# Performance work log

Hardware: AMD Instinct MI355X
Metric: run time of the kernel (lower is better)

## Reference

```python
import jax, jax.numpy as jnp
import numpy as np

BN_EPS = 1e-5
NORM_EPS = 1e-12  # F.normalize default eps


def reference(x, conv_w, bn_gamma, bn_beta):
    # 1x1 conv dimension reduction: [B,2048,H,W] -> [B,256,H,W]
    z = jnp.einsum('bchw,dc->bdhw', x, conv_w)
    # BatchNorm2d (training-mode batch statistics) + ReLU
    mu = z.mean(axis=(0, 2, 3), keepdims=True)
    var = z.var(axis=(0, 2, 3), keepdims=True)
    z = (z - mu) / jnp.sqrt(var + BN_EPS)
    z = z * bn_gamma.reshape(1, -1, 1, 1) + bn_beta.reshape(1, -1, 1, 1)
    z = jax.nn.relu(z)

    B, d, h, w = z.shape
    M = h * w
    xm = z.reshape(B, d, M)
    # Covpool: y = x I_hat x^T with I_hat = (I - 11^T/M)/M == centered 2nd moment
    xc = xm - xm.mean(axis=-1, keepdims=True)
    cov = jnp.einsum('bdm,bem->bde', xc, xc) / M  # [B,d,d]

    # Eigen decomposition (cov is symmetric PSD; SVD of PSD == eigh)
    s, U = jnp.linalg.eigh(cov)  # s: [B,d], U: [B,d,d]
    eps = jnp.finfo(cov.dtype).eps
    s = jnp.maximum(s, eps)

    # ExponentialInverse: U exp(-S) U^T
    inv_x = jnp.einsum('bid,bd,bjd->bij', U, jnp.exp(-s), U)
    # Power (matrix sqrt): U S^{1/2} U^T
    out = jnp.einsum('bid,bd,bjd->bij', U, jnp.sqrt(s), U)

    # attention = out @ inv_x^T  (inv_x is symmetric, transpose kept for fidelity)
    att = jnp.einsum('bij,bkj->bik', out, inv_x)
    flat = att.reshape(B, -1)
    nrm = jnp.maximum(jnp.linalg.norm(flat, axis=1, keepdims=True), NORM_EPS)
    normalized = (flat / nrm).reshape(att.shape)
    att = out * (att / normalized)

    y = att + out
    iu = jnp.triu_indices(d)
    return y[:, iu[0], iu[1]]  # [B, d*(d+1)/2]


def setup_inputs() -> dict:
    key = jax.random.key(0)
    k1, k2 = jax.random.split(key)
    x = jax.random.normal(k1, (32, 2048, 28, 28), dtype=jnp.float32)
    # kaiming-normal fan_out scaling for 1x1 conv: std = sqrt(2/fan_out)=sqrt(2/256)
    conv_w = jax.random.normal(k2, (256, 2048), dtype=jnp.float32) * np.sqrt(2.0 / 256.0)
    bn_gamma = jnp.ones((256,), dtype=jnp.float32)
    bn_beta = jnp.zeros((256,), dtype=jnp.float32)
    return {'x': x, 'conv_w': conv_w, 'bn_gamma': bn_gamma, 'bn_beta': bn_beta}
```

## Files before the change

kernel.cpp:

```cpp
#include <hip/hip_runtime.h>


typedef unsigned short u16;
typedef __attribute__((ext_vector_type(8))) short bf16x8;
typedef __attribute__((ext_vector_type(4))) float f32x4;

__device__ __forceinline__ u16 f2bf(float f) {
  unsigned u = __builtin_bit_cast(unsigned, f);
  u += 0x7FFFu + ((u >> 16) & 1u);
  return (u16)(u >> 16);
}
__device__ __forceinline__ float bf2f(u16 h) {
  unsigned u = ((unsigned)h) << 16;
  return __builtin_bit_cast(float, u);
}

__device__ __forceinline__
void mm_core(const u16* __restrict__ Ah, const u16* __restrict__ Al,
             const u16* __restrict__ Bh, const u16* __restrict__ Bl,
             long boff, int row0, int col0,
             u16 (*lds)[128][8][8], f32x4 acc[4][2])
{
  const int tid = threadIdx.x;
  const int wave = tid >> 6, lane = tid & 63;
  const int wm = wave >> 2, wn = wave & 3;
  const int mL = lane & 15, q = lane >> 4;
  const u16* baseA[2] = {Ah + boff, Al + boff};
  const u16* baseB[2] = {Bh + boff, Bl + boff};

  for (int k0 = 0; k0 < 256; k0 += 64) {
    __syncthreads();
#pragma unroll
    for (int it = 0; it < 8; ++it) {
      const int t = it >> 1;
      const int r = ((it & 1) << 9) + tid;
      const int m = r >> 3, c = r & 7;
      const u16* src = (t < 2 ? baseA[t] : baseB[t - 2])
                     + (long)((t < 2 ? row0 : col0) + m) * 256 + k0 + c * 8;
      *reinterpret_cast<uint4*>(&lds[t][m][c ^ (m & 7)][0]) =
          *reinterpret_cast<const uint4*>(src);
    }
    __syncthreads();
#pragma unroll
    for (int kk = 0; kk < 2; ++kk) {
      bf16x8 ah[4], al[4], bh[2], bl[2];
#pragma unroll
      for (int i = 0; i < 4; ++i) {
        const int ma = wm * 64 + i * 16 + mL;
        const int ca = (kk * 4 + q) ^ (ma & 7);
        ah[i] = *reinterpret_cast<const bf16x8*>(&lds[0][ma][ca][0]);
        al[i] = *reinterpret_cast<const bf16x8*>(&lds[1][ma][ca][0]);
      }
#pragma unroll
      for (int j = 0; j < 2; ++j) {
        const int nb = wn * 32 + j * 16 + mL;
        const int cb = (kk * 4 + q) ^ (nb & 7);
        bh[j] = *reinterpret_cast<const bf16x8*>(&lds[2][nb][cb][0]);
        bl[j] = *reinterpret_cast<const bf16x8*>(&lds[3][nb][cb][0]);
      }
#pragma unroll
      for (int i = 0; i < 4; ++i)
#pragma unroll
        for (int j = 0; j < 2; ++j) {
          acc[i][j] = __builtin_amdgcn_mfma_f32_16x16x32_bf16(ah[i], bh[j], acc[i][j], 0, 0, 0);
          acc[i][j] = __builtin_amdgcn_mfma_f32_16x16x32_bf16(ah[i], bl[j], acc[i][j], 0, 0, 0);
          acc[i][j] = __builtin_amdgcn_mfma_f32_16x16x32_bf16(al[i], bh[j], acc[i][j], 0, 0, 0);
        }
    }
  }
}

template<int MB>
__global__ __launch_bounds__(512)
void fuse_k(const u16* __restrict__ A0, const u16* __restrict__ B0, u16* __restrict__ C0,
            float al0, float b10, float dg0, const float* __restrict__ cf0,
            const u16* __restrict__ A1, const u16* __restrict__ B1, u16* __restrict__ C1,
            u16* __restrict__ D1, float al1, float b11, float dg1,
            float hc1, float hc2, float hc3, const float* __restrict__ cf1, long LO)
{
  __shared__ u16 lds[4][128][8][8];
  int z = blockIdx.z;
  const bool hB = (z >= 32);
  const u16 *Ah, *Bh; u16 *C, *D = nullptr;
  float al, b1, dg; const float* cf;
  if (!hB) { Ah = A0; Bh = B0; C = C0; al = al0; b1 = b10; dg = dg0; cf = cf0; }
  else { z -= 32; Ah = A1; Bh = B1; C = C1; D = D1; al = al1; b1 = b11; dg = dg1; cf = cf1; }
  const long boff = (long)z * 65536;
  const int row0 = blockIdx.y * 128, col0 = blockIdx.x * 128;
  const int wave = threadIdx.x >> 6, lane = threadIdx.x & 63;
  const int wm = wave >> 2, wn = wave & 3;
  const int mL = lane & 15, q = lane >> 4;

  f32x4 acc[4][2];
#pragma unroll
  for (int i = 0; i < 4; ++i)
#pragma unroll
    for (int j = 0; j < 2; ++j) acc[i][j] = {0.f, 0.f, 0.f, 0.f};

  mm_core(Ah, Ah + LO, Bh, Bh + LO, boff, row0, col0, lds, acc);

#pragma unroll
  for (int i = 0; i < 4; ++i) {
    const int rbase = row0 + wm * 64 + i * 16 + q * 4;
#pragma unroll
    for (int j = 0; j < 2; ++j) {
      const int cc = col0 + wn * 32 + j * 16 + mL;
#pragma unroll
      for (int rg = 0; rg < 4; ++rg) {
        const int rr = rbase + rg;
        const long o = boff + (long)rr * 256 + cc;
        const float vr = acc[i][j][rg];
        if (MB == 1 && hB) {
          u16 h = f2bf(vr);
          C[o] = h; C[o + LO] = f2bf(vr - bf2f(h));
          float hv = fmaf(vr, hc1, cf[o] * hc2);
          if (rr == cc) hv += hc3;
          h = f2bf(hv);
          D[o] = h; D[o + LO] = f2bf(hv - bf2f(h));
        } else {
          float v = al * vr;
          if (cf) v = fmaf(b1, cf[o], v);
          if (rr == cc) v += dg;
          const u16 h = f2bf(v);
          C[o] = h; C[o + LO] = f2bf(v - bf2f(h));
        }
      }
    }
  }
}

__global__ __launch_bounds__(512)
void gemm2_pair_k(const u16* __restrict__ A0, const u16* __restrict__ B0, u16* __restrict__ C0,
                  const u16* __restrict__ A1, const u16* __restrict__ B1, u16* __restrict__ C1,
                  long LO)
{
  __shared__ u16 lds[4][128][8][8];
  int z = blockIdx.z;
  const u16 *Ah, *Bh; u16* Chp;
  if (z < 32) { Ah = A0; Bh = B0; Chp = C0; }
  else { z -= 32; Ah = A1; Bh = B1; Chp = C1; }
  const long boff = (long)z * 65536;
  const int row0 = blockIdx.y * 128, col0 = blockIdx.x * 128;
  const int wave = threadIdx.x >> 6, lane = threadIdx.x & 63;
  const int wm = wave >> 2, wn = wave & 3;
  const int mL = lane & 15, q = lane >> 4;

  f32x4 acc[4][2];
#pragma unroll
  for (int i = 0; i < 4; ++i)
#pragma unroll
    for (int j = 0; j < 2; ++j) acc[i][j] = {0.f, 0.f, 0.f, 0.f};

  mm_core(Ah, Ah + LO, Bh, Bh + LO, boff, row0, col0, lds, acc);

#pragma unroll
  for (int i = 0; i < 4; ++i) {
    const int rbase = row0 + wm * 64 + i * 16 + q * 4;
#pragma unroll
    for (int j = 0; j < 2; ++j) {
      const int cc = col0 + wn * 32 + j * 16 + mL;
#pragma unroll
      for (int rg = 0; rg < 4; ++rg) {
        const long o = boff + (long)(rbase + rg) * 256 + cc;
        const float v = acc[i][j][rg];
        const u16 h = f2bf(v);
        Chp[o] = h; Chp[o + LO] = f2bf(v - bf2f(h));
      }
    }
  }
}

template<int MODE>
__global__ __launch_bounds__(512)
void gemmN64_k(const u16* __restrict__ Ah, const u16* __restrict__ Al,
               const u16* __restrict__ Bh, const u16* __restrict__ Bl,
               u16* __restrict__ Ch, u16* __restrict__ Cl,
               const float* __restrict__ cf, float alpha, float b1, float diag,
               float* __restrict__ attn2)
{
  __shared__ u16 ldsA[2][128][8][8];
  __shared__ u16 ldsB[2][64][8][8];
  const long boff = (long)blockIdx.z * 65536;
  const int row0 = blockIdx.y * 128, col0 = blockIdx.x * 64;
  const int tid = threadIdx.x;
  const int wave = tid >> 6, lane = tid & 63;
  const int wm = wave >> 1, wn = wave & 1;
  const int mL = lane & 15, q = lane >> 4;
  const u16* baseA[2] = {Ah + boff, Al + boff};
  const u16* baseB[2] = {Bh + boff, Bl + boff};

  f32x4 acc[2][2];
#pragma unroll
  for (int i = 0; i < 2; ++i)
#pragma unroll
    for (int j = 0; j < 2; ++j) acc[i][j] = {0.f, 0.f, 0.f, 0.f};

  for (int k0 = 0; k0 < 256; k0 += 64) {
    __syncthreads();
#pragma unroll
    for (int it = 0; it < 4; ++it) {
      const int t = it >> 1;
      const int r = ((it & 1) << 9) + tid;
      const int m = r >> 3, c = r & 7;
      *reinterpret_cast<uint4*>(&ldsA[t][m][c ^ (m & 7)][0]) =
          *reinterpret_cast<const uint4*>(baseA[t] + (long)(row0 + m) * 256 + k0 + c * 8);
    }
#pragma unroll
    for (int it = 0; it < 2; ++it) {
      const int m = tid >> 3, c = tid & 7;
      *reinterpret_cast<uint4*>(&ldsB[it][m][c ^ (m & 7)][0]) =
          *reinterpret_cast<const uint4*>(baseB[it] + (long)(col0 + m) * 256 + k0 + c * 8);
    }
    __syncthreads();
#pragma unroll
    for (int kk = 0; kk < 2; ++kk) {
      bf16x8 ah[2], alo[2], bh[2], bl[2];
#pragma unroll
      for (int i = 0; i < 2; ++i) {
        const int ma = wm * 32 + i * 16 + mL;
        const int ca = (kk * 4 + q) ^ (ma & 7);
        ah[i]  = *reinterpret_cast<const bf16x8*>(&ldsA[0][ma][ca][0]);
        alo[i] = *reinterpret_cast<const bf16x8*>(&ldsA[1][ma][ca][0]);
      }
#pragma unroll
      for (int j = 0; j < 2; ++j) {
        const int nb = wn * 32 + j * 16 + mL;
        const int cb = (kk * 4 + q) ^ (nb & 7);
        bh[j] = *reinterpret_cast<const bf16x8*>(&ldsB[0][nb][cb][0]);
        bl[j] = *reinterpret_cast<const bf16x8*>(&ldsB[1][nb][cb][0]);
      }
#pragma unroll
      for (int i = 0; i < 2; ++i)
#pragma unroll
        for (int j = 0; j < 2; ++j) {
          acc[i][j] = __builtin_amdgcn_mfma_f32_16x16x32_bf16(ah[i],  bh[j], acc[i][j], 0, 0, 0);
          acc[i][j] = __builtin_amdgcn_mfma_f32_16x16x32_bf16(ah[i],  bl[j], acc[i][j], 0, 0, 0);
          acc[i][j] = __builtin_amdgcn_mfma_f32_16x16x32_bf16(alo[i], bh[j], acc[i][j], 0, 0, 0);
        }
    }
  }

  if (MODE == 2) {
    float ssum = 0.f;
#pragma unroll
    for (int i = 0; i < 2; ++i)
#pragma unroll
      for (int j = 0; j < 2; ++j)
#pragma unroll
        for (int rg = 0; rg < 4; ++rg) ssum = fmaf(acc[i][j][rg], acc[i][j][rg], ssum);
#pragma unroll
    for (int o = 32; o > 0; o >>= 1) ssum += __shfl_down(ssum, o);
    __syncthreads();
    float* red = (float*)&ldsA[0][0][0][0];
    if (lane == 0) red[wave] = ssum;
    __syncthreads();
    if (tid == 0) {
      float t8 = 0.f;
#pragma unroll
      for (int wv = 0; wv < 8; ++wv) t8 += red[wv];
      atomicAdd(attn2 + blockIdx.z, t8);
    }
    return;
  }

#pragma unroll
  for (int i = 0; i < 2; ++i) {
    const int rbase = row0 + wm * 32 + i * 16 + q * 4;
#pragma unroll
    for (int j = 0; j < 2; ++j) {
      const int cc = col0 + wn * 32 + j * 16 + mL;
#pragma unroll
      for (int rg = 0; rg < 4; ++rg) {
        const int rr = rbase + rg;
        const long o = boff + (long)rr * 256 + cc;
        float v = alpha * acc[i][j][rg];
        if (cf) v = fmaf(b1, cf[o], v);
        if (rr == cc) v += diag;
        const u16 h = f2bf(v);
        Ch[o] = h; Cl[o] = f2bf(v - bf2f(h));
      }
    }
  }
}

__global__ __launch_bounds__(512)
void conv_k(const u16* __restrict__ wb, const float* __restrict__ x,
            float* __restrict__ z0, float* __restrict__ z1)
{
  __shared__ u16 ldsA[256][8][8];
  __shared__ u16 ldsB[64][8][8];
  const int tid = threadIdx.x;
  const int b = blockIdx.z;
  const int n0 = blockIdx.x * 64;
  const int ks = blockIdx.y;
  const int kb0 = ks * 1024;
  const int wave = tid >> 6, lane = tid & 63;
  const int wm = wave >> 1, wn = wave & 1;
  const int mL = lane & 15, q = lane >> 4;
  const float* xb = x + (long)b * 2048 * 784;
  float* zp = (ks == 0 ? z0 : z1);

  f32x4 acc[4][2];
#pragma unroll
  for (int i = 0; i < 4; ++i)
#pragma unroll
    for (int j = 0; j < 2; ++j) acc[i][j] = {0.f, 0.f, 0.f, 0.f};

  const int kc = tid >> 6, nc = tid & 63;
  const int gn = n0 + nc;
  const bool nok = (gn < 784);

  for (int k0 = 0; k0 < 1024; k0 += 64) {
    const int kg = kb0 + k0;
    __syncthreads();
#pragma unroll
    for (int it = 0; it < 4; ++it) {
      const int g = it * 512 + tid;
      const int m = g >> 3, c = g & 7;
      *reinterpret_cast<uint4*>(&ldsA[m][c ^ (m & 7)][0]) =
          *reinterpret_cast<const uint4*>(wb + (long)m * 2048 + kg + c * 8);
    }
    {
      float vv[8];
#pragma unroll
      for (int jk = 0; jk < 8; ++jk)
        vv[jk] = nok ? xb[(long)(kg + kc * 8 + jk) * 784 + gn] : 0.f;
      ushort4 ua, ub;
      ua.x = f2bf(vv[0]); ua.y = f2bf(vv[1]); ua.z = f2bf(vv[2]); ua.w = f2bf(vv[3]);
      ub.x = f2bf(vv[4]); ub.y = f2bf(vv[5]); ub.z = f2bf(vv[6]); ub.w = f2bf(vv[7]);
      const int ch = kc ^ (nc & 7);
      *reinterpret_cast<ushort4*>(&ldsB[nc][ch][0]) = ua;
      *reinterpret_cast<ushort4*>(&ldsB[nc][ch][4]) = ub;
    }
    __syncthreads();
#pragma unroll
    for (int kk = 0; kk < 2; ++kk) {
      bf16x8 af[4], bfv[2];
#pragma unroll
      for (int i = 0; i < 4; ++i) {
        const int ma = wm * 64 + i * 16 + mL;
        af[i] = *reinterpret_cast<const bf16x8*>(&ldsA[ma][(kk * 4 + q) ^ (ma & 7)][0]);
      }
#pragma unroll
      for (int j = 0; j < 2; ++j) {
        const int nb = wn * 32 + j * 16 + mL;
        bfv[j] = *reinterpret_cast<const bf16x8*>(&ldsB[nb][(kk * 4 + q) ^ (nb & 7)][0]);
      }
#pragma unroll
      for (int i = 0; i < 4; ++i)
#pragma unroll
        for (int j = 0; j < 2; ++j)
          acc[i][j] = __builtin_amdgcn_mfma_f32_16x16x32_bf16(af[i], bfv[j], acc[i][j], 0, 0, 0);
    }
  }
#pragma unroll
  for (int i = 0; i < 4; ++i) {
    const int rbase = wm * 64 + i * 16 + q * 4;
#pragma unroll
    for (int j = 0; j < 2; ++j) {
      const int cc = n0 + wn * 32 + j * 16 + mL;
      if (cc >= 784) continue;
#pragma unroll
      for (int rg = 0; rg < 4; ++rg)
        zp[((long)b * 256 + rbase + rg) * 784 + cc] = acc[i][j][rg];
    }
  }
}

__global__ __launch_bounds__(512)
void gram_k(const u16* __restrict__ zb, const float* __restrict__ rs,
            float* __restrict__ cov, u16* __restrict__ C2h, u16* __restrict__ C2l)
{
  __shared__ u16 ldsA[128][8][8];
  __shared__ u16 ldsB[64][8][8];
  const int tid = threadIdx.x;
  const int b = blockIdx.z;
  const int col0 = blockIdx.x * 64, row0 = blockIdx.y * 128;
  const int wave = tid >> 6, lane = tid & 63;
  const int wm = wave >> 1, wn = wave & 1;
  const int mL = lane & 15, q = lane >> 4;
  const u16* zbb = zb + (long)b * 256 * 832;

  f32x4 acc[2][2];
#pragma unroll
  for (int i = 0; i < 2; ++i)
#pragma unroll
    for (int j = 0; j < 2; ++j) acc[i][j] = {0.f, 0.f, 0.f, 0.f};

  for (int k0 = 0; k0 < 832; k0 += 64) {
    __syncthreads();
#pragma unroll
    for (int it = 0; it < 2; ++it) {
      const int r = it * 512 + tid;
      const int m = r >> 3, c = r & 7;
      *reinterpret_cast<uint4*>(&ldsA[m][c ^ (m & 7)][0]) =
          *reinterpret_cast<const uint4*>(zbb + (long)(row0 + m) * 832 + k0 + c * 8);
    }
    {
      const int m = tid >> 3, c = tid & 7;
      *reinterpret_cast<uint4*>(&ldsB[m][c ^ (m & 7)][0]) =
          *reinterpret_cast<const uint4*>(zbb + (long)(col0 + m) * 832 + k0 + c * 8);
    }
    __syncthreads();
#pragma unroll
    for (int kk = 0; kk < 2; ++kk) {
      bf16x8 af[2], bfv[2];
#pragma unroll
      for (int i = 0; i < 2; ++i) {
        const int ma = wm * 32 + i * 16 + mL;
        af[i] = *reinterpret_cast<const bf16x8*>(&ldsA[ma][(kk * 4 + q) ^ (ma & 7)][0]);
      }
#pragma unroll
      for (int j = 0; j < 2; ++j) {
        const int nb = wn * 32 + j * 16 + mL;
        bfv[j] = *reinterpret_cast<const bf16x8*>(&ldsB[nb][(kk * 4 + q) ^ (nb & 7)][0]);
      }
#pragma unroll
      for (int i = 0; i < 2; ++i)
#pragma unroll
        for (int j = 0; j < 2; ++j)
          acc[i][j] = __builtin_amdgcn_mfma_f32_16x16x32_bf16(af[i], bfv[j], acc[i][j], 0, 0, 0);
    }
  }
  const float inv_m = 1.f / 784.f;
#pragma unroll
  for (int i = 0; i < 2; ++i) {
    const int rr0 = row0 + wm * 32 + i * 16 + q * 4;
#pragma unroll
    for (int j = 0; j < 2; ++j) {
      const int cc = col0 + wn * 32 + j * 16 + mL;
      const float mu_c = rs[b * 256 + cc] * inv_m;
#pragma unroll
      for (int rg = 0; rg < 4; ++rg) {
        const int rr = rr0 + rg;
        const float mu_r = rs[b * 256 + rr] * inv_m;
        const long o = ((long)b * 256 + rr) * 256 + cc;
        const float cv = fmaf(acc[i][j][rg], inv_m, -mu_r * mu_c);
        cov[o] = cv;
        const u16 h = f2bf(cv);
        C2h[o] = h; C2l[o] = f2bf(cv - bf2f(h));
      }
    }
  }
}

__global__ __launch_bounds__(256)
void bn_stats_k(const float* __restrict__ z0, const float* __restrict__ z1,
                float* __restrict__ ps, float* __restrict__ pq)
{
  const int d = blockIdx.x, sl = blockIdx.y, t = threadIdx.x;
  const int lane = t & 63, wid = t >> 6;
  __shared__ float ws[4], wq[4];
  float s = 0.f, qq = 0.f;
  for (int b = sl * 4; b < sl * 4 + 4; ++b) {
    const long off = ((long)b * 256 + d) * 784;
    for (int m = t; m < 784; m += 256) {
      const float v = z0[off + m] + z1[off + m];
      s += v; qq = fmaf(v, v, qq);
    }
  }
#pragma unroll
  for (int o = 32; o > 0; o >>= 1) { s += __shfl_down(s, o); qq += __shfl_down(qq, o); }
  if (lane == 0) { ws[wid] = s; wq[wid] = qq; }
  __syncthreads();
  if (t == 0) {
    ps[d * 8 + sl] = ws[0] + ws[1] + ws[2] + ws[3];
    pq[d * 8 + sl] = wq[0] + wq[1] + wq[2] + wq[3];
  }
}

__global__ __launch_bounds__(256)
void bn_apply_k(const float* __restrict__ z0, const float* __restrict__ z1,
                const float* __restrict__ gamma, const float* __restrict__ beta,
                const float* __restrict__ ps, const float* __restrict__ pq,
                u16* __restrict__ zb, float* __restrict__ rs)
{
  const int d = blockIdx.x, b = blockIdx.y, t = threadIdx.x;
  const int lane = t & 63, wid = t >> 6;
  __shared__ float bc[2], ws[4];
  if (t == 0) {
    float sum = 0.f, sq = 0.f;
#pragma unroll
    for (int s8 = 0; s8 < 8; ++s8) { sum += ps[d * 8 + s8]; sq += pq[d * 8 + s8]; }
    const float inv_n = 1.f / 25088.f;
    const float mean = sum * inv_n;
    const float var = sq * inv_n - mean * mean;
    const float sc = gamma[d] * rsqrtf(var + 1e-5f);
    bc[0] = sc; bc[1] = fmaf(-mean, sc, beta[d]);
  }
  __syncthreads();
  const float sc = bc[0], sh = bc[1];
  const long off = ((long)b * 256 + d) * 784;
  u16* qp = zb + ((long)b * 256 + d) * 832;
  float rsum = 0.f;
  for (int m = t; m < 832; m += 256) {
    const float v = (m < 784)
        ? fmaxf(fmaf(z0[off + m] + z1[off + m], sc, sh), 0.f) : 0.f;
    qp[m] = f2bf(v);
    rsum += v;
  }
#pragma unroll
  for (int o = 32; o > 0; o >>= 1) rsum += __shfl_down(rsum, o);
  if (lane == 0) ws[wid] = rsum;
  __syncthreads();
  if (t == 0) rs[b * 256 + d] = ws[0] + ws[1] + ws[2] + ws[3];
}

__global__ __launch_bounds__(1024)
void power_k(const float* __restrict__ cov, float* __restrict__ s,
             float* __restrict__ attn2)
{
  const int b = blockIdx.x, tid = threadIdx.x;
  const int i = tid & 255, g = tid >> 8;
  const float* A = cov + (long)b * 65536;
  __shared__ float v[256];
  __shared__ float part[4][256];
  __shared__ float red[4];
  if (g == 0) v[i] = 1.f;
  __syncthreads();
  float lam = 1.f;
  for (int it = 0; it < 10; ++it) {
    float u = 0.f;
    const int jb = g * 64;
#pragma unroll 8
    for (int j = jb; j < jb + 64; ++j) u = fmaf(A[(long)j * 256 + i], v[j], u);
    part[g][i] = u;
    __syncthreads();
    if (g == 0) {
      u = part[0][i] + part[1][i] + part[2][i] + part[3][i];
      float ss = u * u;
#pragma unroll
      for (int o = 32; o > 0; o >>= 1) ss += __shfl_down(ss, o);
      if ((i & 63) == 0) red[i >> 6] = ss;
    }
    __syncthreads();
    lam = sqrtf(red[0] + red[1] + red[2] + red[3]);
    if (g == 0) v[i] = u / lam;
    __syncthreads();
  }
  if (tid == 0) { s[b] = 1.8f / lam; attn2[b] = 0.f; }
}

__global__ __launch_bounds__(256)
void init_k(const float* __restrict__ cov, const float* __restrict__ s,
            u16* __restrict__ Yh, u16* __restrict__ Yl,
            u16* __restrict__ Th, u16* __restrict__ Tl)
{
  const int b = blockIdx.y, i = blockIdx.x, j = threadIdx.x;
  const long o = ((long)b * 256 + i) * 256 + j;
  const float a = cov[o] * s[b];
  u16 h = f2bf(a);
  Yh[o] = h; Yl[o] = f2bf(a - bf2f(h));
  float tv = -0.5f * a;
  if (i == j) tv += 1.5f;
  h = f2bf(tv);
  Th[o] = h; Tl[o] = f2bf(tv - bf2f(h));
}

__global__ __launch_bounds__(256)
void out_k(const u16* __restrict__ Yh, const u16* __restrict__ Yl,
           const float* __restrict__ s, const float* __restrict__ attn2,
           float* __restrict__ out)
{
  const int i = blockIdx.x, b = blockIdx.y, j = threadIdx.x;
  if (j < i) return;
  const float inv = rsqrtf(s[b]);
  const float nrm = fmaxf(sqrtf(fmaxf(attn2[b], 0.f)) * inv, 1e-12f);
  const float scv = inv * (1.f + nrm);
  const long o = ((long)b * 256 + i) * 256 + j;
  const long off = (long)b * 32896 + (long)i * 256 - (long)i * (i - 1) / 2 + (j - i);
  out[off] = (bf2f(Yh[o]) + bf2f(Yl[o])) * scv;
}

__global__ __launch_bounds__(256)
void cast_w_k(const float* __restrict__ w, u16* __restrict__ wb)
{
  const int idx = blockIdx.x * 256 + threadIdx.x;
  wb[idx] = f2bf(w[idx]);
}

extern "C" void kernel_launch(void* const* d_in, const int* in_sizes, int n_in,
                              void* d_out, int out_size, void* d_ws, size_t ws_size,
                              hipStream_t stream)
{
  const float* x     = (const float*)d_in[0];
  const float* w     = (const float*)d_in[1];
  const float* gamma = (const float*)d_in[2];
  const float* beta  = (const float*)d_in[3];
  float* out = (float*)d_out;

  const long PS = 4194304;
  const long LO = 2097152;
  u16* S[9];
  for (int k = 0; k < 9; ++k) S[k] = (u16*)d_ws + (long)k * PS;
  char* base = (char*)d_ws;
  float* z0  = (float*)(base + 75497472);
  float* z1  = (float*)(base + 101187584);
  u16*   zb  = (u16*)(base + 126877696);
  float* cov = (float*)(base + 140509184);
  u16*   wbuf = (u16*)(base + 140509184);
  float* st  = (float*)(base + 148897792);
  float* sv = st, *attn2 = st + 32, *rs = st + 64;
  float* ps = st + 64 + 8192, *pq = ps + 2048;
  u16 *C2 = S[5], *V = S[6], *Ha = S[7], *Hb = S[8];

  const dim3 blk(256), blk5(512);
  const dim3 gP(2, 2, 64);
  const dim3 gT(4, 2, 32);
  const dim3 gE(256, 32);

  cast_w_k<<<dim3(2048), blk, 0, stream>>>(w, wbuf);
  conv_k<<<dim3(13, 2, 32), blk5, 0, stream>>>(wbuf, x, z0, z1);
  bn_stats_k<<<dim3(256, 8), blk, 0, stream>>>(z0, z1, ps, pq);
  bn_apply_k<<<dim3(256, 32), blk, 0, stream>>>(z0, z1, gamma, beta, ps, pq, zb, rs);
  gram_k<<<gT, blk5, 0, stream>>>(zb, rs, cov, C2, C2 + LO);
  power_k<<<dim3(32), dim3(1024), 0, stream>>>(cov, sv, attn2);
  init_k<<<gE, blk, 0, stream>>>(cov, sv, S[0], S[0] + LO, S[1], S[1] + LO);

  fuse_k<1><<<gP, blk5, 0, stream>>>(
      S[0], S[1], S[2], 1.f, 0.f, 0.f, (const float*)nullptr,
      C2, C2, V, Ha, 1.f, 0.f, 0.f,
      1.f / 40320.f, -1.f / 5040.f, 1.f / 720.f, cov, LO);

  int iY = 2, iZ = 1, fa = 0, fb = 3, fc = 4;
  for (int it = 1; it <= 7; ++it) {
    const int iT = fa;
    if (it == 1)
      fuse_k<0><<<gP, blk5, 0, stream>>>(
          S[iZ], S[iY], S[iT], -0.5f, 0.f, 1.5f, (const float*)nullptr,
          V, Ha, Hb, (u16*)nullptr, 1.f, -1.f / 120.f, 1.f / 24.f,
          0.f, 0.f, 0.f, cov, LO);
    else if (it == 2)
      fuse_k<0><<<gP, blk5, 0, stream>>>(
          S[iZ], S[iY], S[iT], -0.5f, 0.f, 1.5f, (const float*)nullptr,
          V, Hb, Ha, (u16*)nullptr, 1.f, -1.f / 6.f, 0.5f,
          0.f, 0.f, 0.f, cov, LO);
    else if (it == 3)
      fuse_k<0><<<gP, blk5, 0, stream>>>(
          S[iZ], S[iY], S[iT], -0.5f, 0.f, 1.5f, (const float*)nullptr,
          V, Ha, Hb, (u16*)nullptr, 1.f, -1.f, 1.f,
          0.f, 0.f, 0.f, cov, LO);
    else
      gemmN64_k<0><<<gT, blk5, 0, stream>>>(
          S[iZ], S[iZ] + LO, S[iY], S[iY] + LO, S[iT], S[iT] + LO,
          (const float*)nullptr, -0.5f, 0.f, 1.5f, (float*)nullptr);
    if (it < 7) {
      gemm2_pair_k<<<gP, blk5, 0, stream>>>(S[iY], S[iT], S[fb],
                                            S[iT], S[iZ], S[fc], LO);
      const int nY = fb, nZ = fc;
      fa = iY; fb = iZ; fc = iT;
      iY = nY; iZ = nZ;
    } else {
      gemmN64_k<0><<<gT, blk5, 0, stream>>>(
          S[iY], S[iY] + LO, S[iT], S[iT] + LO, S[fb], S[fb] + LO,
          (const float*)nullptr, 1.f, 0.f, 0.f, (float*)nullptr);
      iY = fb;
    }
  }

  gemmN64_k<2><<<gT, blk5, 0, stream>>>(
      S[iY], S[iY] + LO, Hb, Hb + LO, (u16*)nullptr, (u16*)nullptr,
      (const float*)nullptr, 1.f, 0.f, 0.f, attn2);
  out_k<<<gE, blk, 0, stream>>>(S[iY], S[iY] + LO, sv, attn2, out);
}
```

Measured before the change: 681.1 us.

## Shrink fused GEMM tiles, software-pipeline conv gather, vectorize BN kernels

```diff
diff --git a/kernel.cpp b/kernel.cpp
--- a/kernel.cpp
+++ b/kernel.cpp
@@ -15,70 +15,16 @@
   return __builtin_bit_cast(float, u);
 }
 
-__device__ __forceinline__
-void mm_core(const u16* __restrict__ Ah, const u16* __restrict__ Al,
-             const u16* __restrict__ Bh, const u16* __restrict__ Bl,
-             long boff, int row0, int col0,
-             u16 (*lds)[128][8][8], f32x4 acc[4][2])
-{
-  const int tid = threadIdx.x;
-  const int wave = tid >> 6, lane = tid & 63;
-  const int wm = wave >> 2, wn = wave & 3;
-  const int mL = lane & 15, q = lane >> 4;
-  const u16* baseA[2] = {Ah + boff, Al + boff};
-  const u16* baseB[2] = {Bh + boff, Bl + boff};
-
-  for (int k0 = 0; k0 < 256; k0 += 64) {
-    __syncthreads();
-#pragma unroll
-    for (int it = 0; it < 8; ++it) {
-      const int t = it >> 1;
-      const int r = ((it & 1) << 9) + tid;
-      const int m = r >> 3, c = r & 7;
-      const u16* src = (t < 2 ? baseA[t] : baseB[t - 2])
-                     + (long)((t < 2 ? row0 : col0) + m) * 256 + k0 + c * 8;
-      *reinterpret_cast<uint4*>(&lds[t][m][c ^ (m & 7)][0]) =
-          *reinterpret_cast<const uint4*>(src);
-    }
-    __syncthreads();
-#pragma unroll
-    for (int kk = 0; kk < 2; ++kk) {
-      bf16x8 ah[4], al[4], bh[2], bl[2];
-#pragma unroll
-      for (int i = 0; i < 4; ++i) {
-        const int ma = wm * 64 + i * 16 + mL;
-        const int ca = (kk * 4 + q) ^ (ma & 7);
-        ah[i] = *reinterpret_cast<const bf16x8*>(&lds[0][ma][ca][0]);
-        al[i] = *reinterpret_cast<const bf16x8*>(&lds[1][ma][ca][0]);
-      }
-#pragma unroll
-      for (int j = 0; j < 2; ++j) {
-        const int nb = wn * 32 + j * 16 + mL;
-        const int cb = (kk * 4 + q) ^ (nb & 7);
-        bh[j] = *reinterpret_cast<const bf16x8*>(&lds[2][nb][cb][0]);
-        bl[j] = *reinterpret_cast<const bf16x8*>(&lds[3][nb][cb][0]);
-      }
-#pragma unroll
-      for (int i = 0; i < 4; ++i)
-#pragma unroll
-        for (int j = 0; j < 2; ++j) {
-          acc[i][j] = __builtin_amdgcn_mfma_f32_16x16x32_bf16(ah[i], bh[j], acc[i][j], 0, 0, 0);
-          acc[i][j] = __builtin_amdgcn_mfma_f32_16x16x32_bf16(ah[i], bl[j], acc[i][j], 0, 0, 0);
-          acc[i][j] = __builtin_amdgcn_mfma_f32_16x16x32_bf16(al[i], bh[j], acc[i][j], 0, 0, 0);
-        }
-    }
-  }
-}
-
 template<int MB>
 __global__ __launch_bounds__(512)
-void fuse_k(const u16* __restrict__ A0, const u16* __restrict__ B0, u16* __restrict__ C0,
-            float al0, float b10, float dg0, const float* __restrict__ cf0,
-            const u16* __restrict__ A1, const u16* __restrict__ B1, u16* __restrict__ C1,
-            u16* __restrict__ D1, float al1, float b11, float dg1,
-            float hc1, float hc2, float hc3, const float* __restrict__ cf1, long LO)
-{
-  __shared__ u16 lds[4][128][8][8];
+void fuseN64_k(const u16* __restrict__ A0, const u16* __restrict__ B0, u16* __restrict__ C0,
+               float al0, float b10, float dg0, const float* __restrict__ cf0,
+               const u16* __restrict__ A1, const u16* __restrict__ B1, u16* __restrict__ C1,
+               u16* __restrict__ D1, float al1, float b11, float dg1,
+               float hc1, float hc2, float hc3, const float* __restrict__ cf1, long LO)
+{
+  __shared__ u16 ldsA[2][128][8][8];
+  __shared__ u16 ldsB[2][64][8][8];
   int z = blockIdx.z;
   const bool hB = (z >= 32);
   const u16 *Ah, *Bh; u16 *C, *D = nullptr;
@@ -86,22 +32,68 @@
   if (!hB) { Ah = A0; Bh = B0; C = C0; al = al0; b1 = b10; dg = dg0; cf = cf0; }
   else { z -= 32; Ah = A1; Bh = B1; C = C1; D = D1; al = al1; b1 = b11; dg = dg1; cf = cf1; }
   const long boff = (long)z * 65536;
-  const int row0 = blockIdx.y * 128, col0 = blockIdx.x * 128;
-  const int wave = threadIdx.x >> 6, lane = threadIdx.x & 63;
-  const int wm = wave >> 2, wn = wave & 3;
+  const int row0 = blockIdx.y * 128, col0 = blockIdx.x * 64;
+  const int tid = threadIdx.x;
+  const int wave = tid >> 6, lane = tid & 63;
+  const int wm = wave >> 1, wn = wave & 1;
   const int mL = lane & 15, q = lane >> 4;
-
-  f32x4 acc[4][2];
-#pragma unroll
-  for (int i = 0; i < 4; ++i)
+  const u16* baseA[2] = {Ah + boff, Ah + LO + boff};
+  const u16* baseB[2] = {Bh + boff, Bh + LO + boff};
+
+  f32x4 acc[2][2];
+#pragma unroll
+  for (int i = 0; i < 2; ++i)
 #pragma unroll
     for (int j = 0; j < 2; ++j) acc[i][j] = {0.f, 0.f, 0.f, 0.f};
 
-  mm_core(Ah, Ah + LO, Bh, Bh + LO, boff, row0, col0, lds, acc);
-
-#pragma unroll
-  for (int i = 0; i < 4; ++i) {
-    const int rbase = row0 + wm * 64 + i * 16 + q * 4;
+  for (int k0 = 0; k0 < 256; k0 += 64) {
+    __syncthreads();
+#pragma unroll
+    for (int it = 0; it < 4; ++it) {
+      const int t = it >> 1;
+      const int r = ((it & 1) << 9) + tid;
+      const int m = r >> 3, c = r & 7;
+      *reinterpret_cast<uint4*>(&ldsA[t][m][c ^ (m & 7)][0]) =
+          *reinterpret_cast<const uint4*>(baseA[t] + (long)(row0 + m) * 256 + k0 + c * 8);
+    }
+#pragma unroll
+    for (int it = 0; it < 2; ++it) {
+      const int m = tid >> 3, c = tid & 7;
+      *reinterpret_cast<uint4*>(&ldsB[it][m][c ^ (m & 7)][0]) =
+          *reinterpret_cast<const uint4*>(baseB[it] + (long)(col0 + m) * 256 + k0 + c * 8);
+    }
+    __syncthreads();
+#pragma unroll
+    for (int kk = 0; kk < 2; ++kk) {
+      bf16x8 ah[2], alo[2], bh[2], bl[2];
+#pragma unroll
+      for (int i = 0; i < 2; ++i) {
+        const int ma = wm * 32 + i * 16 + mL;
+        const int ca = (kk * 4 + q) ^ (ma & 7);
+        ah[i]  = *reinterpret_cast<const bf16x8*>(&ldsA[0][ma][ca][0]);
+        alo[i] = *reinterpret_cast<const bf16x8*>(&ldsA[1][ma][ca][0]);
+      }
+#pragma unroll
+      for (int j = 0; j < 2; ++j) {
+        const int nb = wn * 32 + j * 16 + mL;
+        const int cb = (kk * 4 + q) ^ (nb & 7);
+        bh[j] = *reinterpret_cast<const bf16x8*>(&ldsB[0][nb][cb][0]);
+        bl[j] = *reinterpret_cast<const bf16x8*>(&ldsB[1][nb][cb][0]);
+      }
+#pragma unroll
+      for (int i = 0; i < 2; ++i)
+#pragma unroll
+        for (int j = 0; j < 2; ++j) {
+          acc[i][j] = __builtin_amdgcn_mfma_f32_16x16x32_bf16(ah[i],  bh[j], acc[i][j], 0, 0, 0);
+          acc[i][j] = __builtin_amdgcn_mfma_f32_16x16x32_bf16(ah[i],  bl[j], acc[i][j], 0, 0, 0);
+          acc[i][j] = __builtin_amdgcn_mfma_f32_16x16x32_bf16(alo[i], bh[j], acc[i][j], 0, 0, 0);
+        }
+    }
+  }
+
+#pragma unroll
+  for (int i = 0; i < 2; ++i) {
+    const int rbase = row0 + wm * 32 + i * 16 + q * 4;
 #pragma unroll
     for (int j = 0; j < 2; ++j) {
       const int cc = col0 + wn * 32 + j * 16 + mL;
@@ -129,47 +121,6 @@
   }
 }
 
-__global__ __launch_bounds__(512)
-void gemm2_pair_k(const u16* __restrict__ A0, const u16* __restrict__ B0, u16* __restrict__ C0,
-                  const u16* __restrict__ A1, const u16* __restrict__ B1, u16* __restrict__ C1,
-                  long LO)
-{
-  __shared__ u16 lds[4][128][8][8];
-  int z = blockIdx.z;
-  const u16 *Ah, *Bh; u16* Chp;
-  if (z < 32) { Ah = A0; Bh = B0; Chp = C0; }
-  else { z -= 32; Ah = A1; Bh = B1; Chp = C1; }
-  const long boff = (long)z * 65536;
-  const int row0 = blockIdx.y * 128, col0 = blockIdx.x * 128;
-  const int wave = threadIdx.x >> 6, lane = threadIdx.x & 63;
-  const int wm = wave >> 2, wn = wave & 3;
-  const int mL = lane & 15, q = lane >> 4;
-
-  f32x4 acc[4][2];
-#pragma unroll
-  for (int i = 0; i < 4; ++i)
-#pragma unroll
-    for (int j = 0; j < 2; ++j) acc[i][j] = {0.f, 0.f, 0.f, 0.f};
-
-  mm_core(Ah, Ah + LO, Bh, Bh + LO, boff, row0, col0, lds, acc);
-
-#pragma unroll
-  for (int i = 0; i < 4; ++i) {
-    const int rbase = row0 + wm * 64 + i * 16 + q * 4;
-#pragma unroll
-    for (int j = 0; j < 2; ++j) {
-      const int cc = col0 + wn * 32 + j * 16 + mL;
-#pragma unroll
-      for (int rg = 0; rg < 4; ++rg) {
-        const long o = boff + (long)(rbase + rg) * 256 + cc;
-        const float v = acc[i][j][rg];
-        const u16 h = f2bf(v);
-        Chp[o] = h; Chp[o + LO] = f2bf(v - bf2f(h));
-      }
-    }
-  }
-}
-
 template<int MODE>
 __global__ __launch_bounds__(512)
 void gemmN64_k(const u16* __restrict__ Ah, const u16* __restrict__ Al,
@@ -292,13 +243,12 @@
   const int tid = threadIdx.x;
   const int b = blockIdx.z;
   const int n0 = blockIdx.x * 64;
-  const int ks = blockIdx.y;
-  const int kb0 = ks * 1024;
+  const int kb0 = blockIdx.y * 1024;
   const int wave = tid >> 6, lane = tid & 63;
   const int wm = wave >> 1, wn = wave & 1;
   const int mL = lane & 15, q = lane >> 4;
   const float* xb = x + (long)b * 2048 * 784;
-  float* zp = (ks == 0 ? z0 : z1);
+  float* zp = (blockIdx.y == 0 ? z0 : z1);
 
   f32x4 acc[4][2];
 #pragma unroll
@@ -309,10 +259,14 @@
   const int kc = tid >> 6, nc = tid & 63;
   const int gn = n0 + nc;
   const bool nok = (gn < 784);
-
-  for (int k0 = 0; k0 < 1024; k0 += 64) {
-    const int kg = kb0 + k0;
-    __syncthreads();
+  const int ch = kc ^ (nc & 7);
+
+  auto GATHER = [&](int kg, float* v) {
+    const float* ps = xb + (long)(kg + kc * 8) * 784 + gn;
+#pragma unroll
+    for (int jk = 0; jk < 8; ++jk) v[jk] = nok ? ps[(long)jk * 784] : 0.f;
+  };
+  auto STAGEA = [&](int kg) {
 #pragma unroll
     for (int it = 0; it < 4; ++it) {
       const int g = it * 512 + tid;
@@ -320,19 +274,15 @@
       *reinterpret_cast<uint4*>(&ldsA[m][c ^ (m & 7)][0]) =
           *reinterpret_cast<const uint4*>(wb + (long)m * 2048 + kg + c * 8);
     }
-    {
-      float vv[8];
-#pragma unroll
-      for (int jk = 0; jk < 8; ++jk)
-        vv[jk] = nok ? xb[(long)(kg + kc * 8 + jk) * 784 + gn] : 0.f;
-      ushort4 ua, ub;
-      ua.x = f2bf(vv[0]); ua.y = f2bf(vv[1]); ua.z = f2bf(vv[2]); ua.w = f2bf(vv[3]);
-      ub.x = f2bf(vv[4]); ub.y = f2bf(vv[5]); ub.z = f2bf(vv[6]); ub.w = f2bf(vv[7]);
-      const int ch = kc ^ (nc & 7);
-      *reinterpret_cast<ushort4*>(&ldsB[nc][ch][0]) = ua;
-      *reinterpret_cast<ushort4*>(&ldsB[nc][ch][4]) = ub;
-    }
-    __syncthreads();
+  };
+  auto WRITEB = [&](const float* v) {
+    ushort4 ua, ub;
+    ua.x = f2bf(v[0]); ua.y = f2bf(v[1]); ua.z = f2bf(v[2]); ua.w = f2bf(v[3]);
+    ub.x = f2bf(v[4]); ub.y = f2bf(v[5]); ub.z = f2bf(v[6]); ub.w = f2bf(v[7]);
+    *reinterpret_cast<ushort4*>(&ldsB[nc][ch][0]) = ua;
+    *reinterpret_cast<ushort4*>(&ldsB[nc][ch][4]) = ub;
+  };
+  auto DOMFMA = [&]() {
 #pragma unroll
     for (int kk = 0; kk < 2; ++kk) {
       bf16x8 af[4], bfv[2];
@@ -352,7 +302,25 @@
         for (int j = 0; j < 2; ++j)
           acc[i][j] = __builtin_amdgcn_mfma_f32_16x16x32_bf16(af[i], bfv[j], acc[i][j], 0, 0, 0);
     }
-  }
+  };
+
+  float va[8], vb2[8];
+  GATHER(kb0, va);
+  for (int k0 = 0; k0 < 1024; k0 += 128) {
+    __syncthreads();
+    STAGEA(kb0 + k0);
+    WRITEB(va);
+    __syncthreads();
+    GATHER(kb0 + k0 + 64, vb2);
+    DOMFMA();
+    __syncthreads();
+    STAGEA(kb0 + k0 + 64);
+    WRITEB(vb2);
+    __syncthreads();
+    if (k0 + 128 < 1024) GATHER(kb0 + k0 + 128, va);
+    DOMFMA();
+  }
+
 #pragma unroll
   for (int i = 0; i < 4; ++i) {
     const int rbase = wm * 64 + i * 16 + q * 4;
@@ -454,9 +422,12 @@
   float s = 0.f, qq = 0.f;
   for (int b = sl * 4; b < sl * 4 + 4; ++b) {
     const long off = ((long)b * 256 + d) * 784;
-    for (int m = t; m < 784; m += 256) {
-      const float v = z0[off + m] + z1[off + m];
-      s += v; qq = fmaf(v, v, qq);
+    for (int q4 = t; q4 < 196; q4 += 256) {
+      const float4 a = *reinterpret_cast<const float4*>(z0 + off + q4 * 4);
+      const float4 c = *reinterpret_cast<const float4*>(z1 + off + q4 * 4);
+      const float v0 = a.x + c.x, v1 = a.y + c.y, v2 = a.z + c.z, v3 = a.w + c.w;
+      s += v0 + v1 + v2 + v3;
+      qq = fmaf(v0, v0, fmaf(v1, v1, fmaf(v2, v2, fmaf(v3, v3, qq))));
     }
   }
 #pragma unroll
@@ -493,11 +464,19 @@
   const long off = ((long)b * 256 + d) * 784;
   u16* qp = zb + ((long)b * 256 + d) * 832;
   float rsum = 0.f;
-  for (int m = t; m < 832; m += 256) {
-    const float v = (m < 784)
-        ? fmaxf(fmaf(z0[off + m] + z1[off + m], sc, sh), 0.f) : 0.f;
-    qp[m] = f2bf(v);
-    rsum += v;
+  for (int q4 = t; q4 < 208; q4 += 256) {
+    ushort4 u = {0, 0, 0, 0};
+    if (q4 < 196) {
+      const float4 a = *reinterpret_cast<const float4*>(z0 + off + q4 * 4);
+      const float4 c = *reinterpret_cast<const float4*>(z1 + off + q4 * 4);
+      const float v0 = fmaxf(fmaf(a.x + c.x, sc, sh), 0.f);
+      const float v1 = fmaxf(fmaf(a.y + c.y, sc, sh), 0.f);
+      const float v2 = fmaxf(fmaf(a.z + c.z, sc, sh), 0.f);
+      const float v3 = fmaxf(fmaf(a.w + c.w, sc, sh), 0.f);
+      u.x = f2bf(v0); u.y = f2bf(v1); u.z = f2bf(v2); u.w = f2bf(v3);
+      rsum += v0 + v1 + v2 + v3;
+    }
+    *reinterpret_cast<ushort4*>(qp + q4 * 4) = u;
   }
 #pragma unroll
   for (int o = 32; o > 0; o >>= 1) rsum += __shfl_down(rsum, o);
@@ -605,9 +584,10 @@
   u16 *C2 = S[5], *V = S[6], *Ha = S[7], *Hb = S[8];
 
   const dim3 blk(256), blk5(512);
-  const dim3 gP(2, 2, 64);
+  const dim3 gF(4, 2, 64);
   const dim3 gT(4, 2, 32);
   const dim3 gE(256, 32);
+  const float* nullf = nullptr;
 
   cast_w_k<<<dim3(2048), blk, 0, stream>>>(w, wbuf);
   conv_k<<<dim3(13, 2, 32), blk5, 0, stream>>>(wbuf, x, z0, z1);
@@ -617,8 +597,8 @@
   power_k<<<dim3(32), dim3(1024), 0, stream>>>(cov, sv, attn2);
   init_k<<<gE, blk, 0, stream>>>(cov, sv, S[0], S[0] + LO, S[1], S[1] + LO);
 
-  fuse_k<1><<<gP, blk5, 0, stream>>>(
-      S[0], S[1], S[2], 1.f, 0.f, 0.f, (const float*)nullptr,
+  fuseN64_k<1><<<gF, blk5, 0, stream>>>(
+      S[0], S[1], S[2], 1.f, 0.f, 0.f, nullf,
       C2, C2, V, Ha, 1.f, 0.f, 0.f,
       1.f / 40320.f, -1.f / 5040.f, 1.f / 720.f, cov, LO);
 
@@ -626,40 +606,42 @@
   for (int it = 1; it <= 7; ++it) {
     const int iT = fa;
     if (it == 1)
-      fuse_k<0><<<gP, blk5, 0, stream>>>(
-          S[iZ], S[iY], S[iT], -0.5f, 0.f, 1.5f, (const float*)nullptr,
+      fuseN64_k<0><<<gF, blk5, 0, stream>>>(
+          S[iZ], S[iY], S[iT], -0.5f, 0.f, 1.5f, nullf,
           V, Ha, Hb, (u16*)nullptr, 1.f, -1.f / 120.f, 1.f / 24.f,
           0.f, 0.f, 0.f, cov, LO);
     else if (it == 2)
-      fuse_k<0><<<gP, blk5, 0, stream>>>(
-          S[iZ], S[iY], S[iT], -0.5f, 0.f, 1.5f, (const float*)nullptr,
+      fuseN64_k<0><<<gF, blk5, 0, stream>>>(
+          S[iZ], S[iY], S[iT], -0.5f, 0.f, 1.5f, nullf,
           V, Hb, Ha, (u16*)nullptr, 1.f, -1.f / 6.f, 0.5f,
           0.f, 0.f, 0.f, cov, LO);
     else if (it == 3)
-      fuse_k<0><<<gP, blk5, 0, stream>>>(
-          S[iZ], S[iY], S[iT], -0.5f, 0.f, 1.5f, (const float*)nullptr,
+      fuseN64_k<0><<<gF, blk5, 0, stream>>>(
+          S[iZ], S[iY], S[iT], -0.5f, 0.f, 1.5f, nullf,
           V, Ha, Hb, (u16*)nullptr, 1.f, -1.f, 1.f,
           0.f, 0.f, 0.f, cov, LO);
     else
       gemmN64_k<0><<<gT, blk5, 0, stream>>>(
           S[iZ], S[iZ] + LO, S[iY], S[iY] + LO, S[iT], S[iT] + LO,
-          (const float*)nullptr, -0.5f, 0.f, 1.5f, (float*)nullptr);
+          nullf, -0.5f, 0.f, 1.5f, (float*)nullptr);
     if (it < 7) {
-      gemm2_pair_k<<<gP, blk5, 0, stream>>>(S[iY], S[iT], S[fb],
-                                            S[iT], S[iZ], S[fc], LO);
+      fuseN64_k<0><<<gF, blk5, 0, stream>>>(
+          S[iY], S[iT], S[fb], 1.f, 0.f, 0.f, nullf,
+          S[iT], S[iZ], S[fc], (u16*)nullptr, 1.f, 0.f, 0.f,
+          0.f, 0.f, 0.f, nullf, LO);
       const int nY = fb, nZ = fc;
       fa = iY; fb = iZ; fc = iT;
       iY = nY; iZ = nZ;
     } else {
       gemmN64_k<0><<<gT, blk5, 0, stream>>>(
           S[iY], S[iY] + LO, S[iT], S[iT] + LO, S[fb], S[fb] + LO,
-          (const float*)nullptr, 1.f, 0.f, 0.f, (float*)nullptr);
+          nullf, 1.f, 0.f, 0.f, (float*)nullptr);
       iY = fb;
     }
   }
 
   gemmN64_k<2><<<gT, blk5, 0, stream>>>(
       S[iY], S[iY] + LO, Hb, Hb + LO, (u16*)nullptr, (u16*)nullptr,
-      (const float*)nullptr, 1.f, 0.f, 0.f, attn2);
+      nullf, 1.f, 0.f, 0.f, attn2);
   out_k<<<gE, blk, 0, stream>>>(S[iY], S[iY] + LO, sv, attn2, out);
 }
```

Measured after the change: 734.3 us. 7.8% more time.
